# Optimization experiments

Measured on AMD Instinct MI355X. Metric: run time of the kernel, lower is better.

The kernel has to match this reference:

```python
import jax, jax.numpy as jnp
import numpy as np

D_MODEL = 1024
N_HEADS = 16
D_HEAD = D_MODEL // N_HEADS
CHUNK = 128
DECAY_RATE = 0.9


def setup_inputs() -> dict:
    key = jax.random.key(0)
    ks = jax.random.split(key, 10)
    B, L, D = 4, 4096, D_MODEL
    s = 1.0 / np.sqrt(D)
    return {
        "x": jax.random.normal(ks[0], (B, L, D), dtype=jnp.float32),
        "Wq": jax.random.normal(ks[1], (D, D), dtype=jnp.float32) * s,
        "bq": jnp.zeros((D,), dtype=jnp.float32),
        "Wk": jax.random.normal(ks[2], (D, D), dtype=jnp.float32) * s,
        "bk": jnp.zeros((D,), dtype=jnp.float32),
        "Wv": jax.random.normal(ks[3], (D, D), dtype=jnp.float32) * s,
        "bv": jnp.zeros((D,), dtype=jnp.float32),
        "Wo": jax.random.normal(ks[4], (D, D), dtype=jnp.float32) * s,
        "bo": jnp.zeros((D,), dtype=jnp.float32),
        "decay": jnp.full((N_HEADS,), DECAY_RATE, dtype=jnp.float32),
    }


def _retention(x, Wq, bq, Wk, bk, Wv, bv, Wo, bo, decay):
    B, L, D = x.shape
    H, Dh, C = N_HEADS, D_HEAD, CHUNK
    nC = L // C
    scale = Dh ** -0.5

    def split_heads(y):
        # [B,L,D] -> [nC, B, H, C, Dh]
        y = y.reshape(B, nC, C, H, Dh)
        return jnp.transpose(y, (1, 0, 3, 2, 4))

    q = split_heads(x @ Wq + bq)
    k = split_heads(x @ Wk + bk)
    v = split_heads(x @ Wv + bv)

    # per-head decay^position factor for query positions within a chunk: [H, C]
    pos = jnp.arange(C, dtype=jnp.float32)
    decay_fac = decay[:, None] ** pos[None, :]

    def step(carry, inp):
        pk, pv = carry            # [B,H,Dh] carried last k/v token
        qc, kc, vc = inp          # [B,H,C,Dh]
        kf = jnp.concatenate([pk[:, :, None], kc], axis=2)  # [B,H,C+1,Dh]
        vf = jnp.concatenate([pv[:, :, None], vc], axis=2)
        scores = jnp.einsum("bhqd,bhkd->bhqk", qc, kf) * scale
        scores = scores * decay_fac[None, :, :, None]
        attn = jax.nn.softmax(scores, axis=-1)
        out = jnp.einsum("bhqk,bhkd->bhqd", attn, vf)
        new_carry = (jax.lax.stop_gradient(kf[:, :, -1]),
                     jax.lax.stop_gradient(vf[:, :, -1]))
        return new_carry, out

    init = (jnp.zeros((B, H, Dh), x.dtype), jnp.zeros((B, H, Dh), x.dtype))
    _, ys = jax.lax.scan(step, init, (q, k, v))  # ys: [nC,B,H,C,Dh]
    out = jnp.transpose(ys, (1, 0, 3, 2, 4)).reshape(B, L, D)
    return out @ Wo + bo


def reference(x, Wq, bq, Wk, bk, Wv, bv, Wo, bo, decay):
    return _retention(x, Wq, bq, Wk, bk, Wv, bv, Wo, bo, decay)
```

## Files before the change

kernel.cpp:

```cpp
#include <hip/hip_runtime.h>

typedef unsigned short u16;
typedef unsigned int   u32;
typedef unsigned long long u64;

typedef __attribute__((ext_vector_type(8))) __bf16 bf16x8;
typedef __attribute__((ext_vector_type(4))) float  floatx4;
typedef __attribute__((ext_vector_type(16))) float floatx16;

#define D_MODEL 1024
#define L_SEQ   4096
#define BATCH   4
#define N_HEADS 16
#define D_HEAD  64
#define CHUNK   128
#define N_CHUNKS 32
#define M_ROWS  (BATCH * L_SEQ)
#define NQKV    3072

__device__ __forceinline__ float bf2f(u16 u) {
    union { u32 i; float f; } x; x.i = ((u32)u) << 16; return x.f;
}
__device__ __forceinline__ u16 f2bf(float f) {
    union { u32 i; float fl; } x; x.fl = f;
    u32 i = x.i;
    u32 r = (i + 0x7FFFu + ((i >> 16) & 1u)) >> 16;
    return (u16)r;
}

__device__ __forceinline__ float load_decay(const void* dec, int h) {
    const u16* d16 = (const u16*)dec;
    const float as_bf = bf2f(d16[0]);
    if (as_bf > 1e-6f && as_bf <= 1.0001f) return bf2f(d16[h]);
    return ((const float*)dec)[h];
}

__device__ __forceinline__ void gload_lds16(const u16* g, u16* l) {
    __builtin_amdgcn_global_load_lds(
        (const __attribute__((address_space(1))) u32*)g,
        (__attribute__((address_space(3))) u32*)l, 16, 0, 0);
}

__global__ void detect_dtypes(const void* __restrict__ x,
                              const void* __restrict__ w,
                              int* __restrict__ flags) {
    const int lane = threadIdx.x;
    const u16* x16 = (const u16*)x;
    const u16* w16 = (const u16*)w;
    const float vx = fabsf(bf2f(x16[lane]));
    const float vw = fabsf(bf2f(w16[lane]));
    const bool ox = (vx != 0.0f) && (vx > 1e4f || vx < 1e-4f);
    const bool ow = (vw != 0.0f) && (vw > 1e4f || vw < 1e-4f);
    const u64 bx = __ballot(ox);
    const u64 bw = __ballot(ow);
    if (lane == 0) {
        flags[0] = (__popcll(bx) >= 8) ? 1 : 0;
        flags[1] = (__popcll(bw) >= 8) ? 1 : 0;
    }
}

__global__ __launch_bounds__(256)
void convert_x(const void* __restrict__ x, const int* __restrict__ flags,
               u16* __restrict__ xb) {
    const int mode = flags[0];
    const size_t i0 = ((size_t)blockIdx.x * 256 + threadIdx.x) * 8;
    if (mode) {
        const float* xf = (const float*)x;
        u16 tmp[8];
#pragma unroll
        for (int j = 0; j < 8; j++) tmp[j] = f2bf(xf[i0 + j]);
        *(uint4*)(xb + i0) = *(const uint4*)tmp;
    } else {
        *(uint4*)(xb + i0) = *(const uint4*)((const u16*)x + i0);
    }
}

__global__ __launch_bounds__(256)
void transpose4(const void* __restrict__ W0, const void* __restrict__ W1,
                const void* __restrict__ W2, const void* __restrict__ W3,
                const int* __restrict__ flags,
                u16* __restrict__ T0, u16* __restrict__ T1,
                u16* __restrict__ T2, u16* __restrict__ T3) {
    __shared__ u16 tile[32][33];
    const int mode = flags[1];
    const void* src; u16* dst;
    switch (blockIdx.z) {
        case 0: src = W0; dst = T0; break;
        case 1: src = W1; dst = T1; break;
        case 2: src = W2; dst = T2; break;
        default: src = W3; dst = T3; break;
    }
    const int tx = threadIdx.x & 31, ty = threadIdx.x >> 5;
    const int x0 = blockIdx.x * 32, y0 = blockIdx.y * 32;
#pragma unroll
    for (int i = 0; i < 32; i += 8) {
        const size_t idx = (size_t)(y0 + ty + i) * D_MODEL + x0 + tx;
        tile[ty + i][tx] = mode ? f2bf(((const float*)src)[idx])
                                : ((const u16*)src)[idx];
    }
    __syncthreads();
#pragma unroll
    for (int i = 0; i < 32; i += 8)
        dst[(size_t)(x0 + ty + i) * D_MODEL + y0 + tx] = tile[tx][ty + i];
}

__global__ __launch_bounds__(256)
void concat_bias(const void* __restrict__ bq, const void* __restrict__ bk,
                 const void* __restrict__ bv, const void* __restrict__ bo,
                 const int* __restrict__ flags, u16* __restrict__ dst) {
    const int i = blockIdx.x * 256 + threadIdx.x;
    const int mode = flags[1];
    const int which = i >> 10, idx = i & 1023;
    const void* src = (which == 0) ? bq : (which == 1) ? bk
                      : (which == 2) ? bv : bo;
    dst[i] = mode ? f2bf(((const float*)src)[idx]) : ((const u16*)src)[idx];
}

template <typename OutT>
__global__ __launch_bounds__(512, 2)
void gemm_256(const u16* __restrict__ A, const u16* __restrict__ Bt,
              const u16* __restrict__ bias, OutT* __restrict__ C, int N) {
    extern __shared__ u16 lds[];
    constexpr int K  = 1024;
    constexpr int NT = K / 64;

    const int t = threadIdx.x;
    const int lane = t & 63, w = t >> 6;
    const int l31 = lane & 31, hi = lane >> 5;
    const int wm = w >> 2, wn = w & 3;

    const int bid = blockIdx.x;
    const int m0 = (((bid & 7) << 3) + ((bid >> 3) & 7)) * 256;
    const int n0 = (bid >> 6) * 256;

    const int rl = lane >> 3;
    const int sseg = (lane & 7) ^ rl;

    auto STAGE_A = [&](int kt, int half) {
        u16* l0 = lds + (kt & 1) * 32768 + (half * 128 + w * 8) * 64;
        const u16* g0 = A + (size_t)(m0 + half * 128 + w * 8 + rl) * K
                          + kt * 64 + sseg * 8;
        gload_lds16(g0, l0);
        gload_lds16(g0 + (size_t)64 * K, l0 + 64 * 64);
    };
    auto STAGE_B = [&](int kt, int half) {
        u16* l0 = lds + (kt & 1) * 32768 + 16384 + (half * 128 + w * 8) * 64;
        const u16* g0 = Bt + (size_t)(n0 + half * 128 + w * 8 + rl) * K
                           + kt * 64 + sseg * 8;
        gload_lds16(g0, l0);
        gload_lds16(g0 + (size_t)64 * K, l0 + 64 * 64);
    };

    bf16x8 af[2][4], bfr[4];
    floatx16 acc[2][2][2];
#pragma unroll
    for (int a = 0; a < 2; a++)
#pragma unroll
        for (int b = 0; b < 2; b++)
#pragma unroll
            for (int i = 0; i < 2; i++)
#pragma unroll
                for (int r = 0; r < 16; r++)
                    acc[a][b][i][r] = 0.f;

    auto LDA = [&](int cur, int mh) {
        const u16* tb = lds + cur * 32768;
#pragma unroll
        for (int i = 0; i < 2; i++) {
            const int row = mh * 128 + wm * 64 + i * 32 + l31;
#pragma unroll
            for (int ks = 0; ks < 4; ks++) {
                const int seg = (ks * 2 + hi) ^ (row & 7);
                af[i][ks] = *(const bf16x8*)(tb + row * 64 + seg * 8);
            }
        }
    };
    auto LDB = [&](int cur, int nh) {
        const u16* tb = lds + cur * 32768 + 16384;
        const int row = nh * 128 + wn * 32 + l31;
#pragma unroll
        for (int ks = 0; ks < 4; ks++) {
            const int seg = (ks * 2 + hi) ^ (row & 7);
            bfr[ks] = *(const bf16x8*)(tb + row * 64 + seg * 8);
        }
    };
    auto MMQ = [&](floatx16 (&aq)[2]) {
        __builtin_amdgcn_s_setprio(1);
#pragma unroll
        for (int i = 0; i < 2; i++)
#pragma unroll
            for (int ks = 0; ks < 4; ks++)
                aq[i] = __builtin_amdgcn_mfma_f32_32x32x16_bf16(
                    af[i][ks], bfr[ks], aq[i], 0, 0, 0);
        __builtin_amdgcn_s_setprio(0);
    };

    STAGE_A(0, 0); STAGE_B(0, 0); STAGE_A(0, 1); STAGE_B(0, 1);
    STAGE_A(1, 0); STAGE_B(1, 1);
    asm volatile("s_waitcnt vmcnt(4)" ::: "memory");
    __builtin_amdgcn_s_barrier();

    for (int kt = 0; kt < NT; ++kt) {
        const int cur = kt & 1;
        LDA(cur, 0); LDB(cur, 0);
        if (kt + 1 < NT) STAGE_A(kt + 1, 1);
        __builtin_amdgcn_s_barrier();
        MMQ(acc[0][0]);
        LDB(cur, 1);
        if (kt + 1 < NT) STAGE_B(kt + 1, 0);
        __builtin_amdgcn_s_barrier();
        MMQ(acc[0][1]);
        LDA(cur, 1);
        if (kt + 2 < NT) STAGE_A(kt + 2, 0);
        __builtin_amdgcn_s_barrier();
        MMQ(acc[1][1]);
        LDB(cur, 0);
        if (kt + 2 < NT) STAGE_B(kt + 2, 1);
        __builtin_amdgcn_s_barrier();
        MMQ(acc[1][0]);
        if (kt + 2 < NT) asm volatile("s_waitcnt vmcnt(4)" ::: "memory");
        else             asm volatile("s_waitcnt vmcnt(0)" ::: "memory");
        __builtin_amdgcn_s_barrier();
    }

    if constexpr (sizeof(OutT) == 2) {
        u16* sm = lds;
#pragma unroll
        for (int mh = 0; mh < 2; mh++) {
            __syncthreads();
#pragma unroll
            for (int nh = 0; nh < 2; nh++) {
                const int lcol = nh * 128 + wn * 32 + l31;
                const float bsf = bf2f(bias[n0 + lcol]);
#pragma unroll
                for (int i = 0; i < 2; i++)
#pragma unroll
                    for (int r = 0; r < 16; r++) {
                        const int srow = wm * 64 + i * 32 +
                                         (r & 3) + 8 * (r >> 2) + 4 * hi;
                        sm[srow * 264 + lcol] = f2bf(acc[mh][nh][i][r] + bsf);
                    }
            }
            __syncthreads();
#pragma unroll
            for (int it = 0; it < 8; it++) {
                const int lin = it * 512 + t;
                const int row = lin >> 5, seg = lin & 31;
                *(uint4*)&C[(size_t)(m0 + mh * 128 + row) * N + n0 + seg * 8] =
                    *(const uint4*)&sm[row * 264 + seg * 8];
            }
        }
    } else {
#pragma unroll
        for (int mh = 0; mh < 2; mh++)
#pragma unroll
            for (int nh = 0; nh < 2; nh++) {
                const int gcol = n0 + nh * 128 + wn * 32 + l31;
                const float bsf = bf2f(bias[gcol]);
#pragma unroll
                for (int i = 0; i < 2; i++)
#pragma unroll
                    for (int r = 0; r < 16; r++) {
                        const int gr = m0 + mh * 128 + wm * 64 + i * 32 +
                                       (r & 3) + 8 * (r >> 2) + 4 * hi;
                        C[(size_t)gr * N + gcol] = acc[mh][nh][i][r] + bsf;
                    }
            }
    }
}

#define QS 72
#define PS 136
#define VT 136
#define OS 72
#define KS_OFF (128 * QS)

__global__ __launch_bounds__(256)
void retention_mfma(const u16* __restrict__ qkv, const void* __restrict__ dec,
                    u16* __restrict__ att) {
    __shared__ u16 qk[2 * 128 * QS];
    __shared__ u16 vt[64 * VT];
    __shared__ float kp[64], vp[64], s0f[128];
    u16* Ps = qk;
    u16* Osm = qk;

    const int c = blockIdx.x, b = blockIdx.y, h = blockIdx.z;
    const int t = threadIdx.x;
    const int lane = t & 63, w = t >> 6;
    const int col16 = lane & 15, quad = lane >> 4;
    const int R0 = w * 32;
    const size_t base  = ((size_t)b * L_SEQ) * NQKV + h * D_HEAD;
    const size_t gbase = base + (size_t)(c * CHUNK) * NQKV;
    const size_t obase = (((size_t)b * L_SEQ) + c * CHUNK) * D_MODEL + h * D_HEAD;

#pragma unroll
    for (int it = 0; it < 4; it++) {
        const int i = it * 256 + t;
        const int row = i >> 3, seg = i & 7;
        const size_t go = gbase + (size_t)row * NQKV + seg * 8;
        *(uint4*)&qk[row * QS + seg * 8]          = *(const uint4*)(qkv + go);
        *(uint4*)&qk[KS_OFF + row * QS + seg * 8] = *(const uint4*)(qkv + go + 1024);
    }
#pragma unroll
    for (int it = 0; it < 4; it++) {
        const int i = it * 256 + t;
        const int key = i & 127, dseg = i >> 7;
        u16 tmp[8];
        *(uint4*)tmp = *(const uint4*)(qkv + gbase + (size_t)key * NQKV + 2048 + dseg * 8);
#pragma unroll
        for (int j = 0; j < 8; j++)
            vt[(dseg * 8 + j) * VT + key] = tmp[j];
    }
    if (t < 64) {
        const int gl = c * CHUNK - 1;
        float kpv = 0.f, vpv = 0.f;
        if (gl >= 0) {
            const size_t go = base + (size_t)gl * NQKV + t;
            kpv = bf2f(qkv[go + 1024]);
            vpv = bf2f(qkv[go + 2048]);
        }
        kp[t] = kpv; vp[t] = vpv;
    }
    __syncthreads();

    {
        const int row = t >> 1, half = t & 1;
        const u16* qrow = &qk[row * QS + half * 32];
        float s = 0.f;
#pragma unroll
        for (int d = 0; d < 32; d++) s += bf2f(qrow[d]) * kp[half * 32 + d];
        s += __shfl_xor(s, 1, 64);
        if (half == 0) s0f[row] = s;
    }
    __syncthreads();

    floatx4 accs[2][8];
#pragma unroll
    for (int rt = 0; rt < 2; rt++)
#pragma unroll
        for (int ct = 0; ct < 8; ct++)
            accs[rt][ct] = floatx4{0.f, 0.f, 0.f, 0.f};

#pragma unroll
    for (int k0 = 0; k0 < 2; k0++) {
        bf16x8 af0 = *(const bf16x8*)&qk[(R0 + col16) * QS + k0 * 32 + quad * 8];
        bf16x8 af1 = *(const bf16x8*)&qk[(R0 + 16 + col16) * QS + k0 * 32 + quad * 8];
#pragma unroll
        for (int ct = 0; ct < 8; ct++) {
            bf16x8 bfr = *(const bf16x8*)&qk[KS_OFF + (ct * 16 + col16) * QS + k0 * 32 + quad * 8];
            accs[0][ct] = __builtin_amdgcn_mfma_f32_16x16x32_bf16(af0, bfr, accs[0][ct], 0, 0, 0);
            accs[1][ct] = __builtin_amdgcn_mfma_f32_16x16x32_bf16(af1, bfr, accs[1][ct], 0, 0, 0);
        }
    }
    __syncthreads();

    const float dval = load_decay(dec, h);
    const float logd = __logf(dval);
    float p0v[2][4], invv[2][4];
#pragma unroll
    for (int rt = 0; rt < 2; rt++) {
#pragma unroll
        for (int r = 0; r < 4; r++) {
            const int row = R0 + rt * 16 + quad * 4 + r;
            const float dp = __expf((float)row * logd) * 0.125f;
            const float s0p = s0f[row] * dp;
            float vals[8];
            float vmax = s0p;
#pragma unroll
            for (int ct = 0; ct < 8; ct++) {
                vals[ct] = accs[rt][ct][r] * dp;
                vmax = fmaxf(vmax, vals[ct]);
            }
#pragma unroll
            for (int off = 1; off < 16; off <<= 1)
                vmax = fmaxf(vmax, __shfl_xor(vmax, off, 64));
            float lsum = 0.f;
#pragma unroll
            for (int ct = 0; ct < 8; ct++) {
                const float e = __expf(vals[ct] - vmax);
                lsum += e;
                Ps[row * PS + ct * 16 + col16] = f2bf(e);
            }
#pragma unroll
            for (int off = 1; off < 16; off <<= 1)
                lsum += __shfl_xor(lsum, off, 64);
            const float p0 = __expf(s0p - vmax);
            p0v[rt][r] = p0;
            invv[rt][r] = 1.0f / (lsum + p0);
        }
    }

    floatx4 acco[2][4];
#pragma unroll
    for (int rt = 0; rt < 2; rt++)
#pragma unroll
        for (int nt = 0; nt < 4; nt++)
            acco[rt][nt] = floatx4{0.f, 0.f, 0.f, 0.f};

#pragma unroll
    for (int k0 = 0; k0 < 4; k0++) {
        bf16x8 af0 = *(const bf16x8*)&Ps[(R0 + col16) * PS + k0 * 32 + quad * 8];
        bf16x8 af1 = *(const bf16x8*)&Ps[(R0 + 16 + col16) * PS + k0 * 32 + quad * 8];
#pragma unroll
        for (int nt = 0; nt < 4; nt++) {
            bf16x8 bfr = *(const bf16x8*)&vt[(nt * 16 + col16) * VT + k0 * 32 + quad * 8];
            acco[0][nt] = __builtin_amdgcn_mfma_f32_16x16x32_bf16(af0, bfr, acco[0][nt], 0, 0, 0);
            acco[1][nt] = __builtin_amdgcn_mfma_f32_16x16x32_bf16(af1, bfr, acco[1][nt], 0, 0, 0);
        }
    }

    __syncthreads();
#pragma unroll
    for (int nt = 0; nt < 4; nt++) {
        const int gcol = nt * 16 + col16;
        const float vpc = vp[gcol];
#pragma unroll
        for (int rt = 0; rt < 2; rt++) {
#pragma unroll
            for (int r = 0; r < 4; r++) {
                const int row = R0 + rt * 16 + quad * 4 + r;
                const float val = (acco[rt][nt][r] + p0v[rt][r] * vpc) * invv[rt][r];
                Osm[row * OS + gcol] = f2bf(val);
            }
        }
    }
    __syncthreads();
#pragma unroll
    for (int it = 0; it < 4; it++) {
        const int lin = it * 256 + t;
        const int row = lin >> 3, seg = lin & 7;
        *(uint4*)&att[obase + (size_t)row * D_MODEL + seg * 8] =
            *(const uint4*)&Osm[row * OS + seg * 8];
    }
}

extern "C" void kernel_launch(void* const* d_in, const int* in_sizes, int n_in,
                              void* d_out, int out_size, void* d_ws, size_t ws_size,
                              hipStream_t stream) {
    const void* x   = d_in[0];
    const void* Wq  = d_in[1];
    const void* bq  = d_in[2];
    const void* Wk  = d_in[3];
    const void* bk  = d_in[4];
    const void* Wv  = d_in[5];
    const void* bv  = d_in[6];
    const void* Wo  = d_in[7];
    const void* bo  = d_in[8];
    const void* dec = d_in[9];
    float* out = (float*)d_out;

    char* ws = (char*)d_ws;
    const size_t mat = (size_t)M_ROWS * D_MODEL * sizeof(u16);
    const size_t wsz = (size_t)D_MODEL * D_MODEL * sizeof(u16);
    u16* xb   = (u16*)(ws);
    u16* qkv  = (u16*)(ws + mat);
    u16* WT   = (u16*)(ws + 4 * mat);
    u16* WoT  = WT + 3 * (size_t)D_MODEL * D_MODEL;
    u16* bias = (u16*)(ws + 4 * mat + 4 * wsz);
    int* flags = (int*)(ws + 4 * mat + 4 * wsz + 8192);

    dim3 tb(256);
    detect_dtypes<<<1, 64, 0, stream>>>(x, Wq, flags);
    convert_x<<<8192, tb, 0, stream>>>(x, flags, xb);
    transpose4<<<dim3(32, 32, 4), tb, 0, stream>>>(
        Wq, Wk, Wv, Wo, flags,
        WT, WT + wsz / 2, WT + wsz, WoT);
    concat_bias<<<16, tb, 0, stream>>>(bq, bk, bv, bo, flags, bias);
    gemm_256<u16><<<dim3(64 * 12), dim3(512), 131072, stream>>>(
        xb, WT, bias, qkv, NQKV);
    retention_mfma<<<dim3(N_CHUNKS, BATCH, N_HEADS), tb, 0, stream>>>(qkv, dec, xb);
    gemm_256<float><<<dim3(64 * 4), dim3(512), 131072, stream>>>(
        xb, WoT, bias + 3072, out, D_MODEL);
}
```

Before: 335.5 us.

## Keep attention probabilities in registers using transposed 32x32 MFMA for retention

Rewrites the per-chunk attention kernel to compute S^T with 32x32x16 MFMAs so each lane owns one query row. The softmax then needs only a single cross-half shuffle, and the bf16 probabilities feed the P·V MFMA through lane shuffles rather than a round-trip through shared memory. This removes the LDS write and read of P and a barrier. It also raises launch bounds to request two blocks per CU, which risks register pressure from holding 64 fp32 scores per lane.

Result: no change. 333.2 us (-0.7%).

```diff
diff --git a/kernel.cpp b/kernel.cpp
--- a/kernel.cpp
+++ b/kernel.cpp
@@ -26,6 +26,9 @@
     u32 i = x.i;
     u32 r = (i + 0x7FFFu + ((i >> 16) & 1u)) >> 16;
     return (u16)r;
+}
+__device__ __forceinline__ u32 pk2(float a, float b) {
+    return (u32)f2bf(a) | ((u32)f2bf(b) << 16);
 }
 
 __device__ __forceinline__ float load_decay(const void* dec, int h) {
@@ -270,25 +273,24 @@
 }
 
 #define QS 72
-#define PS 136
 #define VT 136
 #define OS 72
 #define KS_OFF (128 * QS)
 
-__global__ __launch_bounds__(256)
+__global__ __launch_bounds__(256, 2)
 void retention_mfma(const u16* __restrict__ qkv, const void* __restrict__ dec,
                     u16* __restrict__ att) {
     __shared__ u16 qk[2 * 128 * QS];
     __shared__ u16 vt[64 * VT];
-    __shared__ float kp[64], vp[64], s0f[128];
-    u16* Ps = qk;
+    __shared__ float kp[64], vp[64], s0f[128], p0i[128];
     u16* Osm = qk;
 
     const int c = blockIdx.x, b = blockIdx.y, h = blockIdx.z;
     const int t = threadIdx.x;
     const int lane = t & 63, w = t >> 6;
-    const int col16 = lane & 15, quad = lane >> 4;
+    const int l31 = lane & 31, hi = lane >> 5;
     const int R0 = w * 32;
+    const int q = R0 + l31;
     const size_t base  = ((size_t)b * L_SEQ) * NQKV + h * D_HEAD;
     const size_t gbase = base + (size_t)(c * CHUNK) * NQKV;
     const size_t obase = (((size_t)b * L_SEQ) + c * CHUNK) * D_MODEL + h * D_HEAD;
@@ -334,94 +336,99 @@
     }
     __syncthreads();
 
-    floatx4 accs[2][8];
-#pragma unroll
-    for (int rt = 0; rt < 2; rt++)
-#pragma unroll
-        for (int ct = 0; ct < 8; ct++)
-            accs[rt][ct] = floatx4{0.f, 0.f, 0.f, 0.f};
-
-#pragma unroll
-    for (int k0 = 0; k0 < 2; k0++) {
-        bf16x8 af0 = *(const bf16x8*)&qk[(R0 + col16) * QS + k0 * 32 + quad * 8];
-        bf16x8 af1 = *(const bf16x8*)&qk[(R0 + 16 + col16) * QS + k0 * 32 + quad * 8];
-#pragma unroll
-        for (int ct = 0; ct < 8; ct++) {
-            bf16x8 bfr = *(const bf16x8*)&qk[KS_OFF + (ct * 16 + col16) * QS + k0 * 32 + quad * 8];
-            accs[0][ct] = __builtin_amdgcn_mfma_f32_16x16x32_bf16(af0, bfr, accs[0][ct], 0, 0, 0);
-            accs[1][ct] = __builtin_amdgcn_mfma_f32_16x16x32_bf16(af1, bfr, accs[1][ct], 0, 0, 0);
-        }
-    }
-    __syncthreads();
+    bf16x8 qf[4];
+#pragma unroll
+    for (int dks = 0; dks < 4; dks++)
+        qf[dks] = *(const bf16x8*)&qk[q * QS + dks * 16 + hi * 8];
+
+    floatx16 sacc[4];
+#pragma unroll
+    for (int kt = 0; kt < 4; kt++) {
+#pragma unroll
+        for (int r = 0; r < 16; r++) sacc[kt][r] = 0.f;
+#pragma unroll
+        for (int dks = 0; dks < 4; dks++) {
+            bf16x8 kf = *(const bf16x8*)&qk[KS_OFF + (kt * 32 + l31) * QS
+                                            + dks * 16 + hi * 8];
+            sacc[kt] = __builtin_amdgcn_mfma_f32_32x32x16_bf16(
+                kf, qf[dks], sacc[kt], 0, 0, 0);
+        }
+    }
 
     const float dval = load_decay(dec, h);
     const float logd = __logf(dval);
-    float p0v[2][4], invv[2][4];
-#pragma unroll
-    for (int rt = 0; rt < 2; rt++) {
-#pragma unroll
-        for (int r = 0; r < 4; r++) {
-            const int row = R0 + rt * 16 + quad * 4 + r;
-            const float dp = __expf((float)row * logd) * 0.125f;
-            const float s0p = s0f[row] * dp;
-            float vals[8];
-            float vmax = s0p;
-#pragma unroll
-            for (int ct = 0; ct < 8; ct++) {
-                vals[ct] = accs[rt][ct][r] * dp;
-                vmax = fmaxf(vmax, vals[ct]);
-            }
-#pragma unroll
-            for (int off = 1; off < 16; off <<= 1)
-                vmax = fmaxf(vmax, __shfl_xor(vmax, off, 64));
-            float lsum = 0.f;
-#pragma unroll
-            for (int ct = 0; ct < 8; ct++) {
-                const float e = __expf(vals[ct] - vmax);
-                lsum += e;
-                Ps[row * PS + ct * 16 + col16] = f2bf(e);
-            }
-#pragma unroll
-            for (int off = 1; off < 16; off <<= 1)
-                lsum += __shfl_xor(lsum, off, 64);
-            const float p0 = __expf(s0p - vmax);
-            p0v[rt][r] = p0;
-            invv[rt][r] = 1.0f / (lsum + p0);
-        }
-    }
-
-    floatx4 acco[2][4];
-#pragma unroll
-    for (int rt = 0; rt < 2; rt++)
-#pragma unroll
-        for (int nt = 0; nt < 4; nt++)
-            acco[rt][nt] = floatx4{0.f, 0.f, 0.f, 0.f};
-
-#pragma unroll
-    for (int k0 = 0; k0 < 4; k0++) {
-        bf16x8 af0 = *(const bf16x8*)&Ps[(R0 + col16) * PS + k0 * 32 + quad * 8];
-        bf16x8 af1 = *(const bf16x8*)&Ps[(R0 + 16 + col16) * PS + k0 * 32 + quad * 8];
-#pragma unroll
-        for (int nt = 0; nt < 4; nt++) {
-            bf16x8 bfr = *(const bf16x8*)&vt[(nt * 16 + col16) * VT + k0 * 32 + quad * 8];
-            acco[0][nt] = __builtin_amdgcn_mfma_f32_16x16x32_bf16(af0, bfr, acco[0][nt], 0, 0, 0);
-            acco[1][nt] = __builtin_amdgcn_mfma_f32_16x16x32_bf16(af1, bfr, acco[1][nt], 0, 0, 0);
-        }
-    }
-
-    __syncthreads();
-#pragma unroll
-    for (int nt = 0; nt < 4; nt++) {
-        const int gcol = nt * 16 + col16;
-        const float vpc = vp[gcol];
-#pragma unroll
-        for (int rt = 0; rt < 2; rt++) {
-#pragma unroll
-            for (int r = 0; r < 4; r++) {
-                const int row = R0 + rt * 16 + quad * 4 + r;
-                const float val = (acco[rt][nt][r] + p0v[rt][r] * vpc) * invv[rt][r];
-                Osm[row * OS + gcol] = f2bf(val);
-            }
+    const float dp = __expf((float)q * logd) * 0.125f;
+    const float s0p = s0f[q] * dp;
+
+    float vmax = s0p;
+#pragma unroll
+    for (int kt = 0; kt < 4; kt++)
+#pragma unroll
+        for (int r = 0; r < 16; r++) {
+            const float v = sacc[kt][r] * dp;
+            sacc[kt][r] = v;
+            vmax = fmaxf(vmax, v);
+        }
+    vmax = fmaxf(vmax, __shfl_xor(vmax, 32, 64));
+
+    float lsum = 0.f;
+#pragma unroll
+    for (int kt = 0; kt < 4; kt++)
+#pragma unroll
+        for (int r = 0; r < 16; r++) {
+            const float e = __expf(sacc[kt][r] - vmax);
+            sacc[kt][r] = e;
+            lsum += e;
+        }
+    lsum += __shfl_xor(lsum, 32, 64);
+    const float p0 = __expf(s0p - vmax);
+    const float inv = 1.0f / (lsum + p0);
+#pragma unroll
+    for (int kt = 0; kt < 4; kt++)
+#pragma unroll
+        for (int r = 0; r < 16; r++) sacc[kt][r] *= inv;
+    if (hi == 0) p0i[q] = p0 * inv;
+
+    floatx16 oacc[2];
+#pragma unroll
+    for (int dt = 0; dt < 2; dt++)
+#pragma unroll
+        for (int r = 0; r < 16; r++) oacc[dt][r] = 0.f;
+
+#pragma unroll
+    for (int s = 0; s < 8; s++) {
+        const int kt = s >> 1, rb = (s & 1) * 8;
+        const u32 c0 = pk2(sacc[kt][rb + 0], sacc[kt][rb + 1]);
+        const u32 c1 = pk2(sacc[kt][rb + 2], sacc[kt][rb + 3]);
+        const u32 c2 = pk2(sacc[kt][rb + 4], sacc[kt][rb + 5]);
+        const u32 c3 = pk2(sacc[kt][rb + 6], sacc[kt][rb + 7]);
+        const u32 pc0 = (u32)__shfl_xor((int)c0, 32, 64);
+        const u32 pc1 = (u32)__shfl_xor((int)c1, 32, 64);
+        const u32 pc2 = (u32)__shfl_xor((int)c2, 32, 64);
+        const u32 pc3 = (u32)__shfl_xor((int)c3, 32, 64);
+        union { uint4 u; bf16x8 v; } aw;
+        aw.u.x = hi ? pc2 : c0;
+        aw.u.y = hi ? pc3 : c1;
+        aw.u.z = hi ? c2 : pc0;
+        aw.u.w = hi ? c3 : pc1;
+#pragma unroll
+        for (int dt = 0; dt < 2; dt++) {
+            bf16x8 vf = *(const bf16x8*)&vt[(dt * 32 + l31) * VT
+                                            + s * 16 + hi * 8];
+            oacc[dt] = __builtin_amdgcn_mfma_f32_32x32x16_bf16(
+                aw.v, vf, oacc[dt], 0, 0, 0);
+        }
+    }
+
+#pragma unroll
+    for (int dt = 0; dt < 2; dt++) {
+        const int d = dt * 32 + l31;
+        const float vpc = vp[d];
+#pragma unroll
+        for (int r = 0; r < 16; r++) {
+            const int ql = (r & 3) + 8 * (r >> 2) + 4 * hi;
+            const float val = oacc[dt][r] + p0i[R0 + ql] * vpc;
+            Osm[(R0 + ql) * OS + d] = f2bf(val);
         }
     }
     __syncthreads();
```
